# Kernel optimization log

Measured on AMD Instinct MI355X. Metric: run time of the kernel, lower is better.

## Reference

```python
import jax, jax.numpy as jnp
import numpy as np
import math

D_MODEL = 1024
NUM_HEADS = 16
HEAD_DIM = D_MODEL // NUM_HEADS
CLAMP = 1e9


def setup_inputs() -> dict:
    key = jax.random.key(0)
    k1, k2, k3, k4, k5 = jax.random.split(key, 5)
    B, S = 2, 2048
    x = jax.random.normal(k1, (B, S, D_MODEL), dtype=jnp.float32)
    # torch Linear params, stored as [in, out] (y = x @ W + b)
    s1 = 1.0 / math.sqrt(D_MODEL)
    W_qkv = jax.random.uniform(k2, (D_MODEL, 3 * D_MODEL), jnp.float32, -s1, s1)
    b_qkv = jax.random.uniform(k3, (3 * D_MODEL,), jnp.float32, -s1, s1)
    W_out = jax.random.uniform(k4, (D_MODEL, D_MODEL), jnp.float32, -s1, s1)
    b_out = jax.random.uniform(k5, (D_MODEL,), jnp.float32, -s1, s1)
    return {"x": x, "W_qkv": W_qkv, "b_qkv": b_qkv, "W_out": W_out, "b_out": b_out}


def reference(x, W_qkv, b_qkv, W_out, b_out):
    B, S, D = x.shape
    qkv = x @ W_qkv + b_qkv                       # [B, S, 3*D]
    qkv = qkv.reshape(B, S, NUM_HEADS, 3 * HEAD_DIM).transpose(0, 2, 1, 3)  # [B, H, S, 3*hd]
    q, k, v = jnp.split(qkv, 3, axis=-1)          # each [B, H, S, hd]
    scale = 1.0 / math.sqrt(HEAD_DIM)
    scores = jnp.einsum('bhqd,bhkd->bhqk', q, k) * scale  # [B, H, S, S]
    causal = jnp.tril(jnp.ones((S, S), dtype=bool))
    scores = jnp.where(causal, scores, -jnp.inf)
    scores = jnp.clip(scores, -CLAMP, CLAMP)      # -inf -> -1e9, matching torch clamp
    attn = jax.nn.softmax(scores, axis=-1)
    values = jnp.einsum('bhqk,bhkd->bhqd', attn, v)        # [B, H, S, hd]
    values = values.transpose(0, 2, 1, 3).reshape(B, S, D)  # [B, S, D]
    out = values @ W_out + b_out
    # dropout is identity in eval mode
    return out
```

## Files before the change

### kernel.cpp

```cpp
#include <hip/hip_runtime.h>
#include <hip/hip_bf16.h>

#define D_MODEL 1024
#define NUM_HEADS 16
#define HEAD_DIM 64
#define SEQ 2048
#define BATCH 2
#define ROWS (BATCH * SEQ)

typedef unsigned short u16;
typedef __bf16 bf16x8 __attribute__((ext_vector_type(8)));
typedef float f32x4 __attribute__((ext_vector_type(4)));

__device__ inline u16 f2bfu(float f) {
  unsigned u = __float_as_uint(f);
  unsigned r = (u + 0x7fffu + ((u >> 16) & 1u)) >> 16;
  return (u16)r;
}

__device__ inline unsigned cvt_pk_bf16(float a, float b) {
#if __has_builtin(__builtin_amdgcn_cvt_pk_bf16_f32)
  auto r = __builtin_amdgcn_cvt_pk_bf16_f32(a, b);
  unsigned u;
  __builtin_memcpy(&u, &r, 4);
  return u;
#else
  return (unsigned)f2bfu(a) | ((unsigned)f2bfu(b) << 16);
#endif
}

__device__ inline f32x4 mfma16(bf16x8 a, bf16x8 b, f32x4 c) {
  return __builtin_amdgcn_mfma_f32_16x16x32_bf16(a, b, c, 0, 0, 0);
}

__device__ inline bf16x8 load_frag(const u16* p) {
  union { uint4 v; bf16x8 f; } u;
  u.v = *(const uint4*)p;
  return u.f;
}

__device__ inline void gload_lds16(const u16* g, u16* l) {
  __builtin_amdgcn_global_load_lds((const __attribute__((address_space(1))) void*)g,
                                   (__attribute__((address_space(3))) void*)l, 16, 0, 0);
}


__global__ __launch_bounds__(256) void prep_kernel(const float* __restrict__ x,
                                                   u16* __restrict__ xb,
                                                   const float* __restrict__ Wq,
                                                   u16* __restrict__ WqT,
                                                   const float* __restrict__ Wo,
                                                   u16* __restrict__ WoT) {
  __shared__ float t[32][33];
  const int bid = blockIdx.x;
  if (bid < 4096) {
    int i = bid * 256 + threadIdx.x;
    float4 v = ((const float4*)x)[i];
    uint2 o;
    o.x = cvt_pk_bf16(v.x, v.y);
    o.y = cvt_pk_bf16(v.z, v.w);
    ((uint2*)xb)[i] = o;
    return;
  }
  const float* W;
  u16* Wt;
  int N, tIdx;
  if (bid < 4096 + 3072) { W = Wq; Wt = WqT; N = 3072; tIdx = bid - 4096; }
  else                   { W = Wo; Wt = WoT; N = 1024; tIdx = bid - 7168; }
  const int k0 = (tIdx & 31) * 32, n0 = (tIdx >> 5) * 32;
  const int c = threadIdx.x & 31, r8 = threadIdx.x >> 5;
#pragma unroll
  for (int i = 0; i < 4; i++) {
    int r = r8 + i * 8;
    t[r][c] = W[(size_t)(k0 + r) * N + n0 + c];
  }
  __syncthreads();
#pragma unroll
  for (int i = 0; i < 4; i++) {
    int r = r8 + i * 8;
    Wt[(size_t)(n0 + r) * 1024 + k0 + c] = f2bfu(t[c][r]);
  }
}


__global__ __launch_bounds__(256, 3) void gemm_qkv(const u16* __restrict__ A,
                                                   const u16* __restrict__ Bt,
                                                   const float* __restrict__ bias,
                                                   u16* __restrict__ Qb, u16* __restrict__ Kb,
                                                   u16* __restrict__ Vt) {
  __shared__ u16 lA0[128 * 32], lB0[128 * 32];
  __shared__ u16 lA1[128 * 32], lB1[128 * 32];
  const int tid = threadIdx.x;
  const int wave = tid >> 6, lane = tid & 63, ln = lane & 15, quad = lane >> 4;
  const int lin = blockIdx.y * 24 + blockIdx.x;
  const int reg = lin & 7, idx = lin >> 3;
  const int mr = idx / 12, nr = idx - mr * 12;
  const int m0 = ((reg >> 1) * 8 + mr) * 128;
  const int n0 = (((reg & 1) * 12) + nr) * 128;
  const int wm = (wave & 1) * 64, wn = (wave >> 1) * 64;
  f32x4 acc[4][4] = {};

  auto issue = [&](u16* dA, u16* dB, int k0) {
#pragma unroll
    for (int i = 0; i < 2; ++i) {
      int rb = wave * 2 + i;
      gload_lds16(A + (size_t)(m0 + rb * 16 + ln) * 1024 + k0 + quad * 8, dA + rb * 512);
      gload_lds16(Bt + (size_t)(n0 + rb * 16 + ln) * 1024 + k0 + quad * 8, dB + rb * 512);
    }
  };
  auto compute = [&](const u16* sA, const u16* sB) {
    bf16x8 a[4], b[4];
#pragma unroll
    for (int i = 0; i < 4; ++i) {
      a[i] = load_frag(sA + (wm / 16 + i) * 512 + quad * 128 + ln * 8);
      b[i] = load_frag(sB + (wn / 16 + i) * 512 + quad * 128 + ln * 8);
    }
#pragma unroll
    for (int mt = 0; mt < 4; ++mt)
#pragma unroll
      for (int nt = 0; nt < 4; ++nt) acc[mt][nt] = mfma16(a[mt], b[nt], acc[mt][nt]);
  };

  issue(lA0, lB0, 0);
  for (int p = 0; p < 15; ++p) {
    asm volatile("s_barrier" ::: "memory");
    issue(lA1, lB1, (2 * p + 1) * 32);
    asm volatile("s_waitcnt vmcnt(4)" ::: "memory");
    asm volatile("s_barrier" ::: "memory");
    compute(lA0, lB0);
    asm volatile("s_barrier" ::: "memory");
    issue(lA0, lB0, (2 * p + 2) * 32);
    asm volatile("s_waitcnt vmcnt(4)" ::: "memory");
    asm volatile("s_barrier" ::: "memory");
    compute(lA1, lB1);
  }
  asm volatile("s_barrier" ::: "memory");
  issue(lA1, lB1, 31 * 32);
  asm volatile("s_waitcnt vmcnt(4)" ::: "memory");
  asm volatile("s_barrier" ::: "memory");
  compute(lA0, lB0);
  asm volatile("s_waitcnt vmcnt(0)" ::: "memory");
  asm volatile("s_barrier" ::: "memory");
  compute(lA1, lB1);

#pragma unroll
  for (int mt = 0; mt < 4; ++mt) {
    int row = m0 + wm + mt * 16 + quad * 4;
    int bb = row >> 11, s0 = row & 2047;
#pragma unroll
    for (int nt = 0; nt < 4; ++nt) {
      int col = n0 + wn + nt * 16 + ln;
      float bv = bias[col];
      int h = col / 192, rem = col - h * 192, t3 = rem >> 6, d = rem & 63;
      int bh = bb * NUM_HEADS + h;
      if (t3 == 2) {
        uint2 pk;
        pk.x = cvt_pk_bf16(acc[mt][nt][0] + bv, acc[mt][nt][1] + bv);
        pk.y = cvt_pk_bf16(acc[mt][nt][2] + bv, acc[mt][nt][3] + bv);
        *(uint2*)(Vt + ((size_t)bh * 64 + d) * SEQ + s0) = pk;
      } else {
        u16* dst = (t3 == 0) ? Qb : Kb;
#pragma unroll
        for (int r = 0; r < 4; ++r)
          dst[((size_t)bh * SEQ + s0 + r) * 64 + d] = f2bfu(acc[mt][nt][r] + bv);
      }
    }
  }
}


__global__ __launch_bounds__(512) void attn_kernel(const u16* __restrict__ Qb,
                                                   const u16* __restrict__ Kb,
                                                   const u16* __restrict__ Vt,
                                                   u16* __restrict__ Ob) {
  __shared__ u16 lK[2 * 64 * 64];
  __shared__ u16 lV[2 * 64 * 64];
  __shared__ u16 lP[8][1152];
  const int tid = threadIdx.x;
  const int wave = tid >> 6, lane = tid & 63;
  const int ln = lane & 15, quad = lane >> 4;
  const int lin = blockIdx.y * 16 + blockIdx.x;
  const int xreg = lin & 7, xidx = lin >> 3;
  const int j = xidx & 15;
  const int bh = xreg * 4 + (xidx >> 4);
  const int lo = j, hi = 31 - j;
  const int myt = (wave < 4) ? lo : hi;
  const int q0w = myt * 64 + (wave & 3) * 16;
  const int sD = myt >> 1;
  const int nsup = (hi + 2) >> 1;
  const u16* Qg = Qb + (size_t)bh * SEQ * 64;
  const u16* Kg = Kb + (size_t)bh * SEQ * 64;
  const u16* Vg = Vt + (size_t)bh * 64 * SEQ;
  u16* lPw = lP[wave];

  bf16x8 qf[2];
#pragma unroll
  for (int ks = 0; ks < 2; ++ks)
    qf[ks] = load_frag(Qg + (size_t)(q0w + ln) * 64 + ks * 32 + quad * 8);

  const u16* sp[4];
  u16* dp[4];
  const int sstep = (wave < 4) ? 128 * 64 : 128;
#pragma unroll
  for (int i = 0; i < 4; ++i) {
    int c = wave * 4 + i;
    if (c < 16) {
      int half = c >> 3, cc = c & 7, rb = cc >> 1, kgh = cc & 1;
      sp[i] = Kg + (size_t)(half * 64 + rb * 16 + ln) * 64 + (kgh * 4 + quad) * 8;
      dp[i] = lK + half * 4096 + rb * 1024 + kgh * 512;
    } else {
      int c2 = c - 16, half = c2 >> 3, cc = c2 & 7, rb = cc >> 1, kgh = cc & 1;
      sp[i] = Vg + (size_t)(rb * 16 + ln) * SEQ + half * 64 + (kgh * 4 + quad) * 8;
      dp[i] = lV + half * 4096 + rb * 1024 + kgh * 512;
    }
  }

  f32x4 o[4] = {};
  float m_r = -1e30f;
  float l_r = 0.f;
  const float SC = 0.18033688011112042f;
  const int qq = q0w + ln;

  for (int s = 0; s < nsup; ++s) {
    __syncthreads();
#pragma unroll
    for (int i = 0; i < 4; ++i) { gload_lds16(sp[i], dp[i]); sp[i] += sstep; }
    __syncthreads();

    if (s <= sD) {
      f32x4 sc[2][4] = {};
#pragma unroll
      for (int h = 0; h < 2; ++h)
#pragma unroll
        for (int mt = 0; mt < 4; ++mt)
#pragma unroll
          for (int ks = 0; ks < 2; ++ks) {
            bf16x8 kf = load_frag(lK + h * 4096 + mt * 1024 + (ks * 4 + quad) * 128 + ln * 8);
            sc[h][mt] = mfma16(kf, qf[ks], sc[h][mt]);
          }
      if (s == sD) {
#pragma unroll
        for (int h = 0; h < 2; ++h)
#pragma unroll
          for (int mt = 0; mt < 4; ++mt) {
            int key0 = (2 * s + h) * 64 + mt * 16 + quad * 4;
#pragma unroll
            for (int r = 0; r < 4; ++r)
              if (key0 + r > qq) sc[h][mt][r] = -1e30f;
          }
      }
      float mloc = sc[0][0][0];
#pragma unroll
      for (int h = 0; h < 2; ++h)
#pragma unroll
        for (int mt = 0; mt < 4; ++mt)
#pragma unroll
          for (int r = 0; r < 4; ++r) mloc = fmaxf(mloc, sc[h][mt][r]);
      mloc = fmaxf(mloc, __shfl_xor(mloc, 16));
      mloc = fmaxf(mloc, __shfl_xor(mloc, 32));
      float mnew = fmaxf(m_r, mloc);
      float alpha = __builtin_amdgcn_exp2f((m_r - mnew) * SC);
      float nmsc = -mnew * SC;
      float sum = 0.f;
#pragma unroll
      for (int h = 0; h < 2; ++h)
#pragma unroll
        for (int mt = 0; mt < 4; ++mt)
#pragma unroll
          for (int r = 0; r < 4; ++r) {
            float p = __builtin_amdgcn_exp2f(__builtin_fmaf(sc[h][mt][r], SC, nmsc));
            sc[h][mt][r] = p;
            sum += p;
          }
      sum += __shfl_xor(sum, 16);
      sum += __shfl_xor(sum, 32);
      l_r = l_r * alpha + sum;
      m_r = mnew;
#pragma unroll
      for (int dt = 0; dt < 4; ++dt) o[dt] *= alpha;

#pragma unroll
      for (int h = 0; h < 2; ++h) {
#pragma unroll
        for (int mt = 0; mt < 4; ++mt) {
          uint2 pk;
          pk.x = cvt_pk_bf16(sc[h][mt][0], sc[h][mt][1]);
          pk.y = cvt_pk_bf16(sc[h][mt][2], sc[h][mt][3]);
          int addr = ln * 64 + (((mt * 2 + (quad >> 1)) ^ (ln & 7)) * 8) + (quad & 1) * 4;
          *(uint2*)(lPw + addr) = pk;
        }
        bf16x8 pf[2];
#pragma unroll
        for (int ks = 0; ks < 2; ++ks)
          pf[ks] = load_frag(lPw + ln * 64 + (((ks * 4 + quad) ^ (ln & 7)) * 8));
#pragma unroll
        for (int dt = 0; dt < 4; ++dt)
#pragma unroll
          for (int ks = 0; ks < 2; ++ks) {
            bf16x8 av = load_frag(lV + h * 4096 + dt * 1024 + (ks * 4 + quad) * 128 + ln * 8);
            o[dt] = mfma16(av, pf[ks], o[dt]);
          }
      }
    }
  }

  float inv = 1.f / l_r;
#pragma unroll
  for (int dt = 0; dt < 4; ++dt) {
    uint2 pk;
    pk.x = cvt_pk_bf16(o[dt][0] * inv, o[dt][1] * inv);
    pk.y = cvt_pk_bf16(o[dt][2] * inv, o[dt][3] * inv);
    *(uint2*)(lPw + ln * 72 + dt * 16 + quad * 4) = pk;
  }
  const int b = bh >> 4, h2 = bh & 15;
#pragma unroll
  for (int i = 0; i < 2; ++i) {
    int c = lane + i * 64;
    int qq2 = c >> 3, dg = c & 7;
    uint4 val = *(const uint4*)(lPw + qq2 * 72 + dg * 8);
    *(uint4*)(Ob + ((size_t)b * SEQ + q0w + qq2) * 1024 + h2 * 64 + dg * 8) = val;
  }
}


__global__ __launch_bounds__(256, 3) void gemm_out(const u16* __restrict__ A,
                                                   const u16* __restrict__ Bt,
                                                   const float* __restrict__ bias,
                                                   float* __restrict__ out) {
  __shared__ u16 lA0[128 * 32], lB0[64 * 32];
  __shared__ u16 lA1[128 * 32], lB1[64 * 32];
  const int tid = threadIdx.x;
  const int wave = tid >> 6, lane = tid & 63, ln = lane & 15, quad = lane >> 4;
  const int lin = blockIdx.y * 16 + blockIdx.x;
  const int reg = lin & 7, idx = lin >> 3;
  const int mr = idx >> 3, nr = idx & 7;
  const int m0 = ((reg >> 1) * 8 + mr) * 128;
  const int n0 = (((reg & 1) * 8) + nr) * 64;
  f32x4 acc[2][4] = {};

  auto issue = [&](u16* dA, u16* dB, int k0) {
#pragma unroll
    for (int i = 0; i < 3; ++i) {
      int c = wave * 3 + i;
      if (c < 8) {
        gload_lds16(A + (size_t)(m0 + c * 16 + ln) * 1024 + k0 + quad * 8, dA + c * 512);
      } else {
        int cc = c - 8;
        gload_lds16(Bt + (size_t)(n0 + cc * 16 + ln) * 1024 + k0 + quad * 8, dB + cc * 512);
      }
    }
  };
  auto compute = [&](const u16* sA, const u16* sB) {
    bf16x8 a[2], b[4];
#pragma unroll
    for (int i = 0; i < 2; ++i)
      a[i] = load_frag(sA + (wave * 2 + i) * 512 + quad * 128 + ln * 8);
#pragma unroll
    for (int i = 0; i < 4; ++i)
      b[i] = load_frag(sB + i * 512 + quad * 128 + ln * 8);
#pragma unroll
    for (int mt = 0; mt < 2; ++mt)
#pragma unroll
      for (int nt = 0; nt < 4; ++nt) acc[mt][nt] = mfma16(a[mt], b[nt], acc[mt][nt]);
  };

  issue(lA0, lB0, 0);
  for (int p = 0; p < 15; ++p) {
    asm volatile("s_barrier" ::: "memory");
    issue(lA1, lB1, (2 * p + 1) * 32);
    asm volatile("s_waitcnt vmcnt(3)" ::: "memory");
    asm volatile("s_barrier" ::: "memory");
    compute(lA0, lB0);
    asm volatile("s_barrier" ::: "memory");
    issue(lA0, lB0, (2 * p + 2) * 32);
    asm volatile("s_waitcnt vmcnt(3)" ::: "memory");
    asm volatile("s_barrier" ::: "memory");
    compute(lA1, lB1);
  }
  asm volatile("s_barrier" ::: "memory");
  issue(lA1, lB1, 31 * 32);
  asm volatile("s_waitcnt vmcnt(3)" ::: "memory");
  asm volatile("s_barrier" ::: "memory");
  compute(lA0, lB0);
  asm volatile("s_waitcnt vmcnt(0)" ::: "memory");
  asm volatile("s_barrier" ::: "memory");
  compute(lA1, lB1);

#pragma unroll
  for (int mt = 0; mt < 2; ++mt) {
    int row = m0 + wave * 32 + mt * 16 + quad * 4;
#pragma unroll
    for (int nt = 0; nt < 4; ++nt) {
      int col = n0 + nt * 16 + ln;
      float bv = bias[col];
#pragma unroll
      for (int r = 0; r < 4; ++r)
        out[(size_t)(row + r) * 1024 + col] = acc[mt][nt][r] + bv;
    }
  }
}


extern "C" void kernel_launch(void* const* d_in, const int* in_sizes, int n_in,
                              void* d_out, int out_size, void* d_ws, size_t ws_size,
                              hipStream_t stream) {
  const float* x = (const float*)d_in[0];
  const float* W_qkv = (const float*)d_in[1];
  const float* b_qkv = (const float*)d_in[2];
  const float* W_out = (const float*)d_in[3];
  const float* b_out = (const float*)d_in[4];
  float* out = (float*)d_out;

  char* ws = (char*)d_ws;
  const size_t SZ_XB = (size_t)ROWS * D_MODEL * 2;
  const size_t SZ_WQKVT = (size_t)3 * D_MODEL * D_MODEL * 2;
  const size_t SZ_WOUTT = (size_t)D_MODEL * D_MODEL * 2;
  const size_t SZ_HEADS = (size_t)BATCH * NUM_HEADS * SEQ * HEAD_DIM * 2;
  u16* xb = (u16*)(ws);
  u16* WqkvT = (u16*)(ws + SZ_XB);
  u16* WoutT = (u16*)(ws + SZ_XB + SZ_WQKVT);
  u16* Qb = (u16*)(ws + SZ_XB + SZ_WQKVT + SZ_WOUTT);
  u16* Kb = (u16*)(ws + SZ_XB + SZ_WQKVT + SZ_WOUTT + SZ_HEADS);
  u16* Vt = (u16*)(ws + SZ_XB + SZ_WQKVT + SZ_WOUTT + 2 * SZ_HEADS);
  u16* Ob = (u16*)(ws + SZ_XB + SZ_WQKVT + SZ_WOUTT + 3 * SZ_HEADS);

  prep_kernel<<<dim3(8192), dim3(256), 0, stream>>>(x, xb, W_qkv, WqkvT, W_out, WoutT);
  gemm_qkv<<<dim3(3 * D_MODEL / 128, ROWS / 128), dim3(256), 0, stream>>>(xb, WqkvT, b_qkv,
                                                                          Qb, Kb, Vt);
  attn_kernel<<<dim3(SEQ / 128, BATCH * NUM_HEADS), dim3(512), 0, stream>>>(Qb, Kb, Vt, Ob);
  gemm_out<<<dim3(D_MODEL / 64, ROWS / 128), dim3(256), 0, stream>>>(Ob, WoutT, b_out, out);
}
```

Baseline: 204.3 us.

## Triple-buffer GEMM LDS stages and double-buffer K tiles in attention

Both GEMMs move from two LDS buffers with four barriers per pair of k-steps to three rotating buffers with one barrier per k-step, so global loads run two stages ahead of compute. In the attention kernel the K tile is double-buffered: the next super-block of K is prefetched during the softmax/PV phase, while V is loaded at the top of each iteration without a second barrier. The extra LDS per block may lower occupancy, and the attention sync ordering for V (issued with no wait before use) is fragile.

Result: no change. 202.2 us (-1.0%).

```diff
diff --git a/kernel.cpp b/kernel.cpp
--- a/kernel.cpp
+++ b/kernel.cpp
@@ -88,8 +88,7 @@
                                                    const float* __restrict__ bias,
                                                    u16* __restrict__ Qb, u16* __restrict__ Kb,
                                                    u16* __restrict__ Vt) {
-  __shared__ u16 lA0[128 * 32], lB0[128 * 32];
-  __shared__ u16 lA1[128 * 32], lB1[128 * 32];
+  __shared__ u16 lA[3][128 * 32], lB[3][128 * 32];
   const int tid = threadIdx.x;
   const int wave = tid >> 6, lane = tid & 63, ln = lane & 15, quad = lane >> 4;
   const int lin = blockIdx.y * 24 + blockIdx.x;
@@ -121,27 +120,30 @@
       for (int nt = 0; nt < 4; ++nt) acc[mt][nt] = mfma16(a[mt], b[nt], acc[mt][nt]);
   };
 
-  issue(lA0, lB0, 0);
-  for (int p = 0; p < 15; ++p) {
-    asm volatile("s_barrier" ::: "memory");
-    issue(lA1, lB1, (2 * p + 1) * 32);
-    asm volatile("s_waitcnt vmcnt(4)" ::: "memory");
-    asm volatile("s_barrier" ::: "memory");
-    compute(lA0, lB0);
-    asm volatile("s_barrier" ::: "memory");
-    issue(lA0, lB0, (2 * p + 2) * 32);
-    asm volatile("s_waitcnt vmcnt(4)" ::: "memory");
-    asm volatile("s_barrier" ::: "memory");
-    compute(lA1, lB1);
-  }
-  asm volatile("s_barrier" ::: "memory");
-  issue(lA1, lB1, 31 * 32);
+  issue(lA[0], lB[0], 0);
+  issue(lA[1], lB[1], 32);
   asm volatile("s_waitcnt vmcnt(4)" ::: "memory");
   asm volatile("s_barrier" ::: "memory");
-  compute(lA0, lB0);
+
+  for (int tt = 0; tt < 10; ++tt) {
+    const int t = tt * 3;
+    issue(lA[2], lB[2], (t + 2) * 32);
+    compute(lA[0], lB[0]);
+    asm volatile("s_waitcnt vmcnt(4)" ::: "memory");
+    asm volatile("s_barrier" ::: "memory");
+    issue(lA[0], lB[0], (t + 3) * 32);
+    compute(lA[1], lB[1]);
+    asm volatile("s_waitcnt vmcnt(4)" ::: "memory");
+    asm volatile("s_barrier" ::: "memory");
+    issue(lA[1], lB[1], (t + 4) * 32);
+    compute(lA[2], lB[2]);
+    asm volatile("s_waitcnt vmcnt(4)" ::: "memory");
+    asm volatile("s_barrier" ::: "memory");
+  }
+  compute(lA[0], lB[0]);
   asm volatile("s_waitcnt vmcnt(0)" ::: "memory");
   asm volatile("s_barrier" ::: "memory");
-  compute(lA1, lB1);
+  compute(lA[1], lB[1]);
 
 #pragma unroll
   for (int mt = 0; mt < 4; ++mt) {
@@ -173,7 +175,7 @@
                                                    const u16* __restrict__ Kb,
                                                    const u16* __restrict__ Vt,
                                                    u16* __restrict__ Ob) {
-  __shared__ u16 lK[2 * 64 * 64];
+  __shared__ u16 lK[2 * 2 * 64 * 64];
   __shared__ u16 lV[2 * 64 * 64];
   __shared__ u16 lP[8][1152];
   const int tid = threadIdx.x;
@@ -200,19 +202,21 @@
 
   const u16* sp[4];
   u16* dp[4];
-  const int sstep = (wave < 4) ? 128 * 64 : 128;
 #pragma unroll
   for (int i = 0; i < 4; ++i) {
-    int c = wave * 4 + i;
-    if (c < 16) {
-      int half = c >> 3, cc = c & 7, rb = cc >> 1, kgh = cc & 1;
+    if (wave < 4) {
+      int c = wave * 4 + i, half = c >> 3, cc = c & 7, rb = cc >> 1, kgh = cc & 1;
       sp[i] = Kg + (size_t)(half * 64 + rb * 16 + ln) * 64 + (kgh * 4 + quad) * 8;
       dp[i] = lK + half * 4096 + rb * 1024 + kgh * 512;
     } else {
-      int c2 = c - 16, half = c2 >> 3, cc = c2 & 7, rb = cc >> 1, kgh = cc & 1;
+      int c2 = wave * 4 - 16 + i, half = c2 >> 3, cc = c2 & 7, rb = cc >> 1, kgh = cc & 1;
       sp[i] = Vg + (size_t)(rb * 16 + ln) * SEQ + half * 64 + (kgh * 4 + quad) * 8;
       dp[i] = lV + half * 4096 + rb * 1024 + kgh * 512;
     }
+  }
+  if (wave < 4) {
+#pragma unroll
+    for (int i = 0; i < 4; ++i) gload_lds16(sp[i], dp[i]);
   }
 
   f32x4 o[4] = {};
@@ -223,11 +227,13 @@
 
   for (int s = 0; s < nsup; ++s) {
     __syncthreads();
-#pragma unroll
-    for (int i = 0; i < 4; ++i) { gload_lds16(sp[i], dp[i]); sp[i] += sstep; }
-    __syncthreads();
+    if (wave >= 4) {
+#pragma unroll
+      for (int i = 0; i < 4; ++i) gload_lds16(sp[i] + (size_t)s * 128, dp[i]);
+    }
 
     if (s <= sD) {
+      const u16* lKs = lK + (s & 1) * 8192;
       f32x4 sc[2][4] = {};
 #pragma unroll
       for (int h = 0; h < 2; ++h)
@@ -235,7 +241,7 @@
         for (int mt = 0; mt < 4; ++mt)
 #pragma unroll
           for (int ks = 0; ks < 2; ++ks) {
-            bf16x8 kf = load_frag(lK + h * 4096 + mt * 1024 + (ks * 4 + quad) * 128 + ln * 8);
+            bf16x8 kf = load_frag(lKs + h * 4096 + mt * 1024 + (ks * 4 + quad) * 128 + ln * 8);
             sc[h][mt] = mfma16(kf, qf[ks], sc[h][mt]);
           }
       if (s == sD) {
@@ -279,6 +285,15 @@
 #pragma unroll
       for (int dt = 0; dt < 4; ++dt) o[dt] *= alpha;
 
+      __syncthreads();
+      if (wave < 4 && s + 1 < nsup) {
+        u16* dsl = (u16*)((s + 1) & 1 ? 8192 : 0);
+#pragma unroll
+        for (int i = 0; i < 4; ++i)
+          gload_lds16(sp[i] + (size_t)(s + 1) * (128 * 64), dp[i] + ((s + 1) & 1) * 8192);
+        (void)dsl;
+      }
+
 #pragma unroll
       for (int h = 0; h < 2; ++h) {
 #pragma unroll
@@ -301,6 +316,13 @@
             o[dt] = mfma16(av, pf[ks], o[dt]);
           }
       }
+    } else {
+      __syncthreads();
+      if (wave < 4 && s + 1 < nsup) {
+#pragma unroll
+        for (int i = 0; i < 4; ++i)
+          gload_lds16(sp[i] + (size_t)(s + 1) * (128 * 64), dp[i] + ((s + 1) & 1) * 8192);
+      }
     }
   }
 
@@ -327,8 +349,7 @@
                                                    const u16* __restrict__ Bt,
                                                    const float* __restrict__ bias,
                                                    float* __restrict__ out) {
-  __shared__ u16 lA0[128 * 32], lB0[64 * 32];
-  __shared__ u16 lA1[128 * 32], lB1[64 * 32];
+  __shared__ u16 lA[3][128 * 32], lB[3][64 * 32];
   const int tid = threadIdx.x;
   const int wave = tid >> 6, lane = tid & 63, ln = lane & 15, quad = lane >> 4;
   const int lin = blockIdx.y * 16 + blockIdx.x;
@@ -364,27 +385,30 @@
       for (int nt = 0; nt < 4; ++nt) acc[mt][nt] = mfma16(a[mt], b[nt], acc[mt][nt]);
   };
 
-  issue(lA0, lB0, 0);
-  for (int p = 0; p < 15; ++p) {
-    asm volatile("s_barrier" ::: "memory");
-    issue(lA1, lB1, (2 * p + 1) * 32);
-    asm volatile("s_waitcnt vmcnt(3)" ::: "memory");
-    asm volatile("s_barrier" ::: "memory");
-    compute(lA0, lB0);
-    asm volatile("s_barrier" ::: "memory");
-    issue(lA0, lB0, (2 * p + 2) * 32);
-    asm volatile("s_waitcnt vmcnt(3)" ::: "memory");
-    asm volatile("s_barrier" ::: "memory");
-    compute(lA1, lB1);
-  }
-  asm volatile("s_barrier" ::: "memory");
-  issue(lA1, lB1, 31 * 32);
+  issue(lA[0], lB[0], 0);
+  issue(lA[1], lB[1], 32);
   asm volatile("s_waitcnt vmcnt(3)" ::: "memory");
   asm volatile("s_barrier" ::: "memory");
-  compute(lA0, lB0);
+
+  for (int tt = 0; tt < 10; ++tt) {
+    const int t = tt * 3;
+    issue(lA[2], lB[2], (t + 2) * 32);
+    compute(lA[0], lB[0]);
+    asm volatile("s_waitcnt vmcnt(3)" ::: "memory");
+    asm volatile("s_barrier" ::: "memory");
+    issue(lA[0], lB[0], (t + 3) * 32);
+    compute(lA[1], lB[1]);
+    asm volatile("s_waitcnt vmcnt(3)" ::: "memory");
+    asm volatile("s_barrier" ::: "memory");
+    issue(lA[1], lB[1], (t + 4) * 32);
+    compute(lA[2], lB[2]);
+    asm volatile("s_waitcnt vmcnt(3)" ::: "memory");
+    asm volatile("s_barrier" ::: "memory");
+  }
+  compute(lA[0], lB[0]);
   asm volatile("s_waitcnt vmcnt(0)" ::: "memory");
   asm volatile("s_barrier" ::: "memory");
-  compute(lA1, lB1);
+  compute(lA[1], lB[1]);
 
 #pragma unroll
   for (int mt = 0; mt < 2; ++mt) {
```
